# Optimization experiments

Hardware: AMD Instinct MI355X
Metric: run time of the kernel (lower is better)

## Reference

```python
import jax, jax.numpy as jnp
import numpy as np

INPUT_DIM, DK, DV = 1024, 128, 128


def setup_inputs() -> dict:
    key = jax.random.key(0)
    ks = jax.random.split(key, 7)
    s = 0.02
    return {
        "x": jax.random.normal(ks[0], (4, 4096, INPUT_DIM), dtype=jnp.float32),
        "Wq": jax.random.normal(ks[1], (INPUT_DIM, DK), dtype=jnp.float32) * s,
        "bq": jnp.zeros((DK,), dtype=jnp.float32),
        "Wk": jax.random.normal(ks[2], (INPUT_DIM, DK), dtype=jnp.float32) * s,
        "bk": jnp.zeros((DK,), dtype=jnp.float32),
        "Wv": jax.random.normal(ks[3], (INPUT_DIM, DV), dtype=jnp.float32) * s,
        "bv": jnp.zeros((DV,), dtype=jnp.float32),
    }


def reference(x, Wq, bq, Wk, bk, Wv, bv):
    # single-head self-attention with explicit QK^T softmax V
    scale = DK ** (-0.5)
    q = x @ Wq + bq          # [b, s, dk]
    k = x @ Wk + bk          # [b, s, dk]
    v = x @ Wv + bv          # [b, s, dv]
    scores = jnp.einsum("bqd,bkd->bqk", q, k) * scale  # [b, s, s]
    attn = jax.nn.softmax(scores, axis=-1)
    return jnp.einsum("bqk,bkd->bqd", attn, v)  # [b, s, dv]
```

## Files before the change

kernel.cpp:

```cpp
#include <hip/hip_runtime.h>
#include <hip/hip_bf16.h>
#include <math.h>
#include <stdint.h>


#define SM_SCALE2 0.1275310225216245f

using f32x4  = __attribute__((ext_vector_type(4))) float;
using f32x16 = __attribute__((ext_vector_type(16))) float;
using bf16x8 = __attribute__((ext_vector_type(8))) short;
using s16x4  = __attribute__((ext_vector_type(4))) short;

#define GLD16(gp, lp) __builtin_amdgcn_global_load_lds(                      \
    (const __attribute__((address_space(1))) void*)(gp),                     \
    (__attribute__((address_space(3))) void*)(lp), 16, 0, 0)

__device__ __forceinline__ short f2bf(float f) {
  union { __hip_bfloat16 h; short s; } u;
  u.h = __float2bfloat16(f);
  return u.s;
}

__global__ __launch_bounds__(256) void wprep_k(const float* __restrict__ Wq,
                                               const float* __restrict__ Wk,
                                               const float* __restrict__ Wv,
                                               short* __restrict__ Wt) {
  int tid = blockIdx.x * 256 + threadIdx.x;
  int mat = tid >> 17;
  int r   = tid & 131071;
  int k   = r >> 7;
  int col = r & 127;
  const float* W = (mat == 0) ? Wq : ((mat == 1) ? Wk : Wv);
  Wt[mat * 131072 + col * 1024 + k] = f2bf(W[k * 128 + col]);
}

__global__ __launch_bounds__(256) void proj_k(const float* __restrict__ x,
                                              const short* __restrict__ Wt,
                                              const float* __restrict__ bq,
                                              const float* __restrict__ bk,
                                              const float* __restrict__ bv,
                                              short* __restrict__ Qb,
                                              short* __restrict__ Kb,
                                              short* __restrict__ Vt) {
  const int r0  = blockIdx.x * 64;
  const int tid  = threadIdx.x;
  const int lane = tid & 63;
  const int w    = tid >> 6;
  const int g    = lane >> 4;
  const int l15  = lane & 15;

  __shared__ __align__(16) char smem[114688];
  const char* Wtb = (const char*)Wt;

  f32x4 acc[3][4][2];
  #pragma unroll
  for (int m = 0; m < 3; ++m)
    #pragma unroll
    for (int rb = 0; rb < 4; ++rb)
      #pragma unroll
      for (int cb = 0; cb < 2; ++cb) acc[m][rb][cb] = (f32x4){0.f, 0.f, 0.f, 0.f};

  const int xrow = tid >> 2;

  {
    char* xs0 = smem;
    char* wt0 = smem + 16384;
    #pragma unroll
    for (int p = 0; p < 4; ++p) {
      const int s = (tid & 3) + 4 * p;
      const float4 v = *(const float4*)(x + (size_t)(r0 + xrow) * 1024 + s * 4);
      s16x4 h = { f2bf(v.x), f2bf(v.y), f2bf(v.z), f2bf(v.w) };
      *(s16x4*)(xs0 + xrow * 128 + (((s >> 1) ^ (xrow & 7)) << 4) + ((s & 1) << 3)) = h;
    }
    #pragma unroll
    for (int m = 0; m < 3; ++m)
      #pragma unroll
      for (int c = 0; c < 4; ++c) {
        const int om = w * 4096 + c * 1024 + lane * 16;
        const int cr = om >> 7;
        const int cb = (om >> 4) & 7;
        GLD16(Wtb + m * 262144 + (size_t)cr * 2048 + ((cb ^ (cr & 7)) << 4),
              wt0 + m * 16384 + w * 4096 + c * 1024);
      }
  }
  __syncthreads();

  for (int t = 0; t < 16; ++t) {
    const int cur = t & 1;
    float4 fx[4];
    if (t < 15) {
      #pragma unroll
      for (int p = 0; p < 4; ++p) {
        const int s = (tid & 3) + 4 * p;
        fx[p] = *(const float4*)(x + (size_t)(r0 + xrow) * 1024 + (t + 1) * 64 + s * 4);
      }
      char* wtn = smem + 16384 + (cur ^ 1) * 49152;
      #pragma unroll
      for (int m = 0; m < 3; ++m)
        #pragma unroll
        for (int c = 0; c < 4; ++c) {
          const int om = w * 4096 + c * 1024 + lane * 16;
          const int cr = om >> 7;
          const int cb = (om >> 4) & 7;
          GLD16(Wtb + m * 262144 + (size_t)cr * 2048 + (t + 1) * 128 + ((cb ^ (cr & 7)) << 4),
                wtn + m * 16384 + w * 4096 + c * 1024);
        }
    }

    const char* xb = smem + cur * 8192;
    const char* wb = smem + 16384 + cur * 49152;
    #pragma unroll
    for (int kc = 0; kc < 2; ++kc) {
      bf16x8 a[4];
      #pragma unroll
      for (int rb = 0; rb < 4; ++rb)
        a[rb] = *(const bf16x8*)(xb + (rb * 16 + l15) * 128 +
                                 ((((kc << 2) + g) ^ (l15 & 7)) << 4));
      #pragma unroll
      for (int m = 0; m < 3; ++m)
        #pragma unroll
        for (int cb = 0; cb < 2; ++cb) {
          const int col = w * 32 + cb * 16 + l15;
          bf16x8 b = *(const bf16x8*)(wb + m * 16384 + col * 128 +
                                      ((((kc << 2) + g) ^ (l15 & 7)) << 4));
          #pragma unroll
          for (int rb = 0; rb < 4; ++rb)
            acc[m][rb][cb] = __builtin_amdgcn_mfma_f32_16x16x32_bf16(a[rb], b,
                                                                     acc[m][rb][cb], 0, 0, 0);
        }
    }

    if (t < 15) {
      char* xsn = smem + (cur ^ 1) * 8192;
      #pragma unroll
      for (int p = 0; p < 4; ++p) {
        const int s = (tid & 3) + 4 * p;
        s16x4 h = { f2bf(fx[p].x), f2bf(fx[p].y), f2bf(fx[p].z), f2bf(fx[p].w) };
        *(s16x4*)(xsn + xrow * 128 + (((s >> 1) ^ (xrow & 7)) << 4) + ((s & 1) << 3)) = h;
      }
    }
    __syncthreads();
  }

  #pragma unroll
  for (int m = 0; m < 2; ++m) {
    short* dst = (m == 0) ? Qb : Kb;
    const float* bias = (m == 0) ? bq : bk;
    #pragma unroll
    for (int cb = 0; cb < 2; ++cb) {
      const int col = w * 32 + cb * 16 + l15;
      const float bc = bias[col];
      #pragma unroll
      for (int rb = 0; rb < 4; ++rb)
        #pragma unroll
        for (int r = 0; r < 4; ++r) {
          float v = acc[m][rb][cb][r] + bc;
          if (m == 0) v *= SM_SCALE2;
          dst[(size_t)(r0 + rb * 16 + (g << 2) + r) * 128 + col] = f2bf(v);
        }
    }
  }
  {
    short* tb = (short*)smem;
    #pragma unroll
    for (int cb = 0; cb < 2; ++cb) {
      const int col = w * 32 + cb * 16 + l15;
      const float bc = bv[col];
      #pragma unroll
      for (int rb = 0; rb < 4; ++rb)
        #pragma unroll
        for (int r = 0; r < 4; ++r)
          tb[col * 72 + rb * 16 + (g << 2) + r] = f2bf(acc[2][rb][cb][r] + bc);
    }
    __syncthreads();
    const int bb = r0 >> 12;
    const int s0 = r0 & 4095;
    const int d  = tid >> 1;
    #pragma unroll
    for (int j = 0; j < 4; ++j) {
      uint4 vd = *(const uint4*)((char*)tb + d * 144 + (tid & 1) * 64 + j * 16);
      *(uint4*)((char*)Vt +
                ((size_t)(bb * 128 + d) * 4096 + s0 + (tid & 1) * 32 + j * 8) * 2) = vd;
    }
  }
}

__global__ __launch_bounds__(256, 2) void attn_part_k(
    const short* __restrict__ Qb, const short* __restrict__ Kb,
    const short* __restrict__ Vt, float* __restrict__ part,
    float2* __restrict__ ml, float* __restrict__ out, int ns, int direct) {
  const int nwg  = gridDim.x;
  const int bid  = blockIdx.x;
  const int orig = (bid & 7) * (nwg >> 3) + (bid >> 3);
  const int split = orig >> 7;
  const int qb    = orig & 127;
  const int nkt   = 64 / ns;
  const int kt0   = split * nkt;

  const int tid  = threadIdx.x;
  const int lane = tid & 63;
  const int w    = tid >> 6;
  const int l31  = lane & 31;
  const bool hi  = lane >= 32;

  __shared__ __align__(16) char smem[65536];

  const int bb = qb >> 5;
  const size_t qg = (size_t)qb * 128 + w * 32 + l31;

  const char* Kg = (const char*)(Kb + ((size_t)bb << 19));
  const char* Vg = (const char*)(Vt + ((size_t)bb << 19));

  bf16x8 qf[8];
  {
    const short* qp = Qb + qg * 128;
    #pragma unroll
    for (int kd = 0; kd < 8; ++kd)
      qf[kd] = *(const bf16x8*)(qp + 16 * kd + (hi ? 8 : 0));
  }

  float m = -__builtin_inff(), lsum = 0.f;
  f32x16 oacc[4];
  #pragma unroll
  for (int dt = 0; dt < 4; ++dt) oacc[dt] = (f32x16)(0.0f);

#define STAGE(BUF, KT) do {                                                   \
    char* kb_ = smem + (BUF) * 32768;                                         \
    char* vb_ = kb_ + 16384;                                                  \
    _Pragma("unroll")                                                         \
    for (int c = 0; c < 4; ++c) {                                             \
      const int o   = w * 4096 + c * 1024 + lane * 16;                        \
      const int kr  = o >> 8;                                                 \
      const int kc_ = (o >> 4) & 15;                                          \
      GLD16(Kg + (size_t)((KT) * 64 + kr) * 256 + ((kc_ ^ (kr & 15)) << 4),   \
            kb_ + w * 4096 + c * 1024);                                       \
      const int dr  = o >> 7;                                                 \
      const int dc_ = (o >> 4) & 7;                                           \
      GLD16(Vg + (size_t)dr * 8192 + (size_t)(KT) * 128 + ((dc_ ^ (dr & 7)) << 4), \
            vb_ + w * 4096 + c * 1024);                                       \
    }                                                                         \
  } while (0)

  STAGE(0, kt0);
  __syncthreads();

  for (int t = 0; t < nkt; ++t) {
    const int cur = t & 1;
    if (t + 1 < nkt) STAGE(cur ^ 1, kt0 + t + 1);

    const char* KT_ = smem + cur * 32768;
    const char* VT_ = KT_ + 16384;

    f32x16 s0 = (f32x16)(0.0f), s1 = (f32x16)(0.0f);
    __builtin_amdgcn_s_setprio(1);
    #pragma unroll
    for (int kd = 0; kd < 8; ++kd) {
      const int ch = (((2 * kd + (hi ? 1 : 0)) ^ (l31 & 15)) << 4);
      bf16x8 k0 = *(const bf16x8*)(KT_ + l31 * 256 + ch);
      bf16x8 k1 = *(const bf16x8*)(KT_ + (32 + l31) * 256 + ch);
      s0 = __builtin_amdgcn_mfma_f32_32x32x16_bf16(k0, qf[kd], s0, 0, 0, 0);
      s1 = __builtin_amdgcn_mfma_f32_32x32x16_bf16(k1, qf[kd], s1, 0, 0, 0);
    }
    __builtin_amdgcn_s_setprio(0);

    float mx = s0[0];
    #pragma unroll
    for (int i = 1; i < 16; ++i) mx = fmaxf(mx, s0[i]);
    #pragma unroll
    for (int i = 0; i < 16; ++i) mx = fmaxf(mx, s1[i]);
    mx = fmaxf(mx, __shfl_xor(mx, 32));
    if (!__all(mx - m <= 8.f)) {
      const float mn = fmaxf(m, mx);
      const float al = exp2f(m - mn);
      m = mn;
      lsum *= al;
      #pragma unroll
      for (int dt = 0; dt < 4; ++dt)
        #pragma unroll
        for (int i = 0; i < 16; ++i) oacc[dt][i] *= al;
    }
    float rs = 0.f;
    #pragma unroll
    for (int i = 0; i < 16; ++i) { s0[i] = exp2f(s0[i] - m); rs += s0[i]; }
    #pragma unroll
    for (int i = 0; i < 16; ++i) { s1[i] = exp2f(s1[i] - m); rs += s1[i]; }
    rs += __shfl_xor(rs, 32);
    lsum += rs;

    unsigned int W[2][4][2];
    #pragma unroll
    for (int rho = 0; rho < 4; ++rho)
      #pragma unroll
      for (int rh = 0; rh < 2; ++rh) {
        asm("v_cvt_pk_bf16_f32 %0, %1, %2"
            : "=v"(W[0][rho][rh]) : "v"(s0[4 * rho + 2 * rh]), "v"(s0[4 * rho + 2 * rh + 1]));
        asm("v_cvt_pk_bf16_f32 %0, %1, %2"
            : "=v"(W[1][rho][rh]) : "v"(s1[4 * rho + 2 * rh]), "v"(s1[4 * rho + 2 * rh + 1]));
      }

    #pragma unroll
    for (int ks = 0; ks < 4; ++ks) {
      const int t2 = ks >> 1, ksl = ks & 1;
      const unsigned int wl0 = W[t2][2 * ksl][0],     wl1 = W[t2][2 * ksl][1];
      const unsigned int wh0 = W[t2][2 * ksl + 1][0], wh1 = W[t2][2 * ksl + 1][1];
      const unsigned int r0 = __shfl_xor(hi ? wl0 : wh0, 32);
      const unsigned int r1 = __shfl_xor(hi ? wl1 : wh1, 32);
      union { unsigned int u[4]; bf16x8 v; } pb;
      pb.u[0] = hi ? r0 : wl0;
      pb.u[1] = hi ? r1 : wl1;
      pb.u[2] = hi ? wh0 : r0;
      pb.u[3] = hi ? wh1 : r1;
      __builtin_amdgcn_s_setprio(1);
      #pragma unroll
      for (int dt = 0; dt < 4; ++dt) {
        const int row = 32 * dt + l31;
        bf16x8 vf = *(const bf16x8*)(VT_ + row * 128 +
                                     (((2 * ks + (hi ? 1 : 0)) ^ (row & 7)) << 4));
        oacc[dt] = __builtin_amdgcn_mfma_f32_32x32x16_bf16(vf, pb.v, oacc[dt], 0, 0, 0);
      }
      __builtin_amdgcn_s_setprio(0);
    }

    __syncthreads();
  }
#undef STAGE

  const float sc = direct ? (1.f / lsum) : 1.f;
  float* dst = direct ? (out + qg * 128)
                      : (part + ((size_t)split * 16384 + qg) * 128);
  #pragma unroll
  for (int dt = 0; dt < 4; ++dt)
    #pragma unroll
    for (int rq = 0; rq < 4; ++rq) {
      f32x4 v = { oacc[dt][4 * rq + 0] * sc, oacc[dt][4 * rq + 1] * sc,
                  oacc[dt][4 * rq + 2] * sc, oacc[dt][4 * rq + 3] * sc };
      *(f32x4*)(dst + dt * 32 + rq * 8 + (hi ? 4 : 0)) = v;
    }
  if (!direct && lane < 32)
    ml[(size_t)split * 16384 + qg] = make_float2(m, lsum);
}

__global__ __launch_bounds__(256) void merge_k(const float* __restrict__ part,
                                               const float2* __restrict__ ml,
                                               float* __restrict__ out, int ns) {
  const int idx = blockIdx.x * 256 + threadIdx.x;
  const int row = idx >> 5;
  const int c4  = idx & 31;

  float M = -__builtin_inff();
  for (int s = 0; s < ns; ++s) M = fmaxf(M, ml[s * 16384 + row].x);
  float L = 0.f;
  for (int s = 0; s < ns; ++s) {
    const float2 v = ml[s * 16384 + row];
    L += v.y * exp2f(v.x - M);
  }
  const float invL = 1.f / L;

  f32x4 o = (f32x4){0.f, 0.f, 0.f, 0.f};
  for (int s = 0; s < ns; ++s) {
    const float wgt = exp2f(ml[s * 16384 + row].x - M) * invL;
    const f32x4 a = *(const f32x4*)(part + ((size_t)s * 16384 + row) * 128 + c4 * 4);
    o += a * wgt;
  }
  *(f32x4*)(out + (size_t)row * 128 + c4 * 4) = o;
}

extern "C" void kernel_launch(void* const* d_in, const int* in_sizes, int n_in,
                              void* d_out, int out_size, void* d_ws, size_t ws_size,
                              hipStream_t stream) {
  (void)in_sizes; (void)n_in; (void)out_size;
  const float* x  = (const float*)d_in[0];
  const float* Wq = (const float*)d_in[1];
  const float* bq = (const float*)d_in[2];
  const float* Wk = (const float*)d_in[3];
  const float* bk = (const float*)d_in[4];
  const float* Wv = (const float*)d_in[5];
  const float* bv = (const float*)d_in[6];
  float* out = (float*)d_out;

  char* ws = (char*)d_ws;
  short* Wt = (short*)ws;
  short* Qb = (short*)(ws + 786432);
  short* Kb = (short*)(ws + 786432 + 4194304);
  short* Vt = (short*)(ws + 786432 + 2 * 4194304);
  const size_t base = 786432 + 3ull * 4194304;

  const size_t per_split = 16384ull * 128 * 4 + 16384ull * 8;
  int ns = 0;
  if (ws_size >= base + 4 * per_split)      ns = 4;
  else if (ws_size >= base + 2 * per_split) ns = 2;
  const int direct = (ns == 0);
  if (direct) ns = 1;

  float*  part = (float*)(ws + base);
  float2* mlp  = (float2*)(ws + base + (size_t)ns * 16384ull * 128 * 4);

  wprep_k<<<dim3(1536), dim3(256), 0, stream>>>(Wq, Wk, Wv, Wt);
  proj_k<<<dim3(256), dim3(256), 0, stream>>>(x, Wt, bq, bk, bv, Qb, Kb, Vt);
  attn_part_k<<<dim3(128 * ns), dim3(256), 0, stream>>>(Qb, Kb, Vt, part, mlp, out,
                                                        ns, direct);
  if (!direct)
    merge_k<<<dim3(2048), dim3(256), 0, stream>>>(part, mlp, out, ns);
}
```

Baseline: 102.3 us.

## Halve projection K-tile to 32 and relayout LDS to cut shared memory

The QKV projection kernel now steps through K in 32-wide tiles over 32 iterations instead of 64-wide over 16, halving the double-buffered LDS footprint (about 114KB down to about 57KB). The XOR swizzle is replaced by a padded x layout (72-byte row stride) and a K-group-major weight layout. The aim is to fit two blocks per CU for more latency hiding. In exchange it doubles the number of barriers and loop iterations, and each global_load_lds chunk is smaller.

Measured after the change: 115.4 us. 1.13x slower.

```diff
diff --git a/kernel.cpp b/kernel.cpp
--- a/kernel.cpp
+++ b/kernel.cpp
@@ -49,7 +49,7 @@
   const int g    = lane >> 4;
   const int l15  = lane & 15;
 
-  __shared__ __align__(16) char smem[114688];
+  __shared__ __align__(16) char smem[58368];
   const char* Wtb = (const char*)Wt;
 
   f32x4 acc[3][4][2];
@@ -61,86 +61,81 @@
       for (int cb = 0; cb < 2; ++cb) acc[m][rb][cb] = (f32x4){0.f, 0.f, 0.f, 0.f};
 
   const int xrow = tid >> 2;
+  const int xsl  = tid & 3;
+
+#define XS(BUF) (smem + (BUF) * 4608)
+#define WTB(BUF) (smem + 9216 + (BUF) * 24576)
+
+#define STAGE_WT(BUF, T) do {                                                 \
+    char* dstb = WTB(BUF);                                                    \
+    _Pragma("unroll")                                                         \
+    for (int c = 0; c < 6; ++c) {                                             \
+      const int o   = c * 4096 + tid * 16;                                    \
+      const int mt  = o >> 13;                                                \
+      const int r_  = o & 8191;                                               \
+      const int gg  = r_ >> 11;                                               \
+      const int col = (r_ >> 4) & 127;                                        \
+      GLD16(Wtb + mt * 262144 + col * 2048 + (T) * 64 + gg * 16, dstb + o);   \
+    }                                                                         \
+  } while (0)
 
   {
-    char* xs0 = smem;
-    char* wt0 = smem + 16384;
-    #pragma unroll
-    for (int p = 0; p < 4; ++p) {
-      const int s = (tid & 3) + 4 * p;
+    char* xs0 = XS(0);
+    #pragma unroll
+    for (int p = 0; p < 2; ++p) {
+      const int s = xsl + 4 * p;
       const float4 v = *(const float4*)(x + (size_t)(r0 + xrow) * 1024 + s * 4);
       s16x4 h = { f2bf(v.x), f2bf(v.y), f2bf(v.z), f2bf(v.w) };
-      *(s16x4*)(xs0 + xrow * 128 + (((s >> 1) ^ (xrow & 7)) << 4) + ((s & 1) << 3)) = h;
-    }
+      *(s16x4*)(xs0 + xrow * 72 + s * 8) = h;
+    }
+    STAGE_WT(0, 0);
+  }
+  __syncthreads();
+
+  for (int t = 0; t < 32; ++t) {
+    const int cur = t & 1;
+    float4 fx[2];
+    if (t < 31) {
+      #pragma unroll
+      for (int p = 0; p < 2; ++p) {
+        const int s = xsl + 4 * p;
+        fx[p] = *(const float4*)(x + (size_t)(r0 + xrow) * 1024 + (t + 1) * 32 + s * 4);
+      }
+      STAGE_WT(cur ^ 1, t + 1);
+    }
+
+    const char* xb = XS(cur);
+    const char* wb = WTB(cur);
+    bf16x8 a[4];
+    #pragma unroll
+    for (int rb = 0; rb < 4; ++rb)
+      a[rb] = *(const bf16x8*)(xb + (rb * 16 + l15) * 72 + g * 16);
     #pragma unroll
     for (int m = 0; m < 3; ++m)
       #pragma unroll
-      for (int c = 0; c < 4; ++c) {
-        const int om = w * 4096 + c * 1024 + lane * 16;
-        const int cr = om >> 7;
-        const int cb = (om >> 4) & 7;
-        GLD16(Wtb + m * 262144 + (size_t)cr * 2048 + ((cb ^ (cr & 7)) << 4),
-              wt0 + m * 16384 + w * 4096 + c * 1024);
-      }
-  }
-  __syncthreads();
-
-  for (int t = 0; t < 16; ++t) {
-    const int cur = t & 1;
-    float4 fx[4];
-    if (t < 15) {
-      #pragma unroll
-      for (int p = 0; p < 4; ++p) {
-        const int s = (tid & 3) + 4 * p;
-        fx[p] = *(const float4*)(x + (size_t)(r0 + xrow) * 1024 + (t + 1) * 64 + s * 4);
-      }
-      char* wtn = smem + 16384 + (cur ^ 1) * 49152;
-      #pragma unroll
-      for (int m = 0; m < 3; ++m)
+      for (int cb = 0; cb < 2; ++cb) {
+        const int col = w * 32 + cb * 16 + l15;
+        bf16x8 b = *(const bf16x8*)(wb + m * 8192 + g * 2048 + col * 16);
         #pragma unroll
-        for (int c = 0; c < 4; ++c) {
-          const int om = w * 4096 + c * 1024 + lane * 16;
-          const int cr = om >> 7;
-          const int cb = (om >> 4) & 7;
-          GLD16(Wtb + m * 262144 + (size_t)cr * 2048 + (t + 1) * 128 + ((cb ^ (cr & 7)) << 4),
-                wtn + m * 16384 + w * 4096 + c * 1024);
-        }
-    }
-
-    const char* xb = smem + cur * 8192;
-    const char* wb = smem + 16384 + cur * 49152;
-    #pragma unroll
-    for (int kc = 0; kc < 2; ++kc) {
-      bf16x8 a[4];
-      #pragma unroll
-      for (int rb = 0; rb < 4; ++rb)
-        a[rb] = *(const bf16x8*)(xb + (rb * 16 + l15) * 128 +
-                                 ((((kc << 2) + g) ^ (l15 & 7)) << 4));
-      #pragma unroll
-      for (int m = 0; m < 3; ++m)
-        #pragma unroll
-        for (int cb = 0; cb < 2; ++cb) {
-          const int col = w * 32 + cb * 16 + l15;
-          bf16x8 b = *(const bf16x8*)(wb + m * 16384 + col * 128 +
-                                      ((((kc << 2) + g) ^ (l15 & 7)) << 4));
-          #pragma unroll
-          for (int rb = 0; rb < 4; ++rb)
-            acc[m][rb][cb] = __builtin_amdgcn_mfma_f32_16x16x32_bf16(a[rb], b,
-                                                                     acc[m][rb][cb], 0, 0, 0);
-        }
-    }
-
-    if (t < 15) {
-      char* xsn = smem + (cur ^ 1) * 8192;
-      #pragma unroll
-      for (int p = 0; p < 4; ++p) {
-        const int s = (tid & 3) + 4 * p;
+        for (int rb = 0; rb < 4; ++rb)
+          acc[m][rb][cb] = __builtin_amdgcn_mfma_f32_16x16x32_bf16(a[rb], b,
+                                                                   acc[m][rb][cb], 0, 0, 0);
+      }
+
+    if (t < 31) {
+      char* xsn = XS(cur ^ 1);
+      #pragma unroll
+      for (int p = 0; p < 2; ++p) {
+        const int s = xsl + 4 * p;
         s16x4 h = { f2bf(fx[p].x), f2bf(fx[p].y), f2bf(fx[p].z), f2bf(fx[p].w) };
-        *(s16x4*)(xsn + xrow * 128 + (((s >> 1) ^ (xrow & 7)) << 4) + ((s & 1) << 3)) = h;
+        *(s16x4*)(xsn + xrow * 72 + s * 8) = h;
       }
     }
     __syncthreads();
   }
+#undef STAGE_WT
+#undef XS
+#undef WTB
 
   #pragma unroll
   for (int m = 0; m < 2; ++m) {
```
